# Kernel optimization log

Measured on AMD Instinct MI355X. Metric: run time of the kernel, lower is better.

The kernel has to match this reference:

```python
import jax, jax.numpy as jnp
import numpy as np

N, K, D, H, F = 4, 2048, 512, 8, 2048
Dh = D // H  # per-head dim_q = dim_v = dim_out = 64
EPS = 1e-10


def _uinit(k, shape, fan_sum):
    c = (6.0 / fan_sum) ** 0.5
    return jax.random.uniform(k, shape, jnp.float32, -c, c)


def setup_inputs() -> dict:
    key = jax.random.key(0)
    ks = jax.random.split(key, 8)
    x = jax.random.normal(ks[0], (N, K, D), jnp.float32)
    # per-head projection weights, stacked over heads: (H, D, Dh)
    Wq = _uinit(ks[1], (H, D, Dh), D + Dh)
    Wk = _uinit(ks[2], (H, D, Dh), D + Dh)
    Wv = _uinit(ks[3], (H, D, Dh), D + Dh)
    bq = jnp.zeros((H, Dh), jnp.float32)
    bk = jnp.zeros((H, Dh), jnp.float32)
    bv = jnp.zeros((H, Dh), jnp.float32)
    Wo = _uinit(ks[4], (H * Dh, D), H * Dh + D)
    bo = jnp.zeros((D,), jnp.float32)
    W1 = _uinit(ks[5], (D, F), D + F)
    b1 = jnp.zeros((F,), jnp.float32)
    W2 = _uinit(ks[6], (F, D), F + D)
    b2 = jnp.zeros((D,), jnp.float32)
    g1 = jnp.ones((D,), jnp.float32)
    be1 = jnp.zeros((D,), jnp.float32)
    g2 = jnp.ones((D,), jnp.float32)
    be2 = jnp.zeros((D,), jnp.float32)
    # causal mask: True = masked position (masked_fill semantics)
    mask = jnp.broadcast_to(jnp.triu(jnp.ones((K, K), bool), 1), (N, K, K))
    return dict(x=x, Wq=Wq, bq=bq, Wk=Wk, bk=bk, Wv=Wv, bv=bv, Wo=Wo, bo=bo,
                W1=W1, b1=b1, W2=W2, b2=b2, g1=g1, be1=be1, g2=g2, be2=be2,
                mask=mask)


def _layer_norm(x, g, b):
    m = x.mean(-1, keepdims=True)
    v = ((x - m) ** 2).mean(-1, keepdims=True)
    return g * (x - m) / jnp.sqrt(v + EPS) + b


def _block(x, Wq, bq, Wk, bk, Wv, bv, Wo, bo, W1, b1, W2, b2, g1, be1, g2, be2, mask):
    # per-head projections: (N, H, K, Dh)
    q = jnp.einsum('nkd,hde->nhke', x, Wq) + bq[None, :, None, :]
    k = jnp.einsum('nkd,hde->nhke', x, Wk) + bk[None, :, None, :]
    v = jnp.einsum('nkd,hde->nhke', x, Wv) + bv[None, :, None, :]
    # full score matrix (N, H, K, K) -- faithful to bmm-softmax-bmm
    s = jnp.einsum('nhqe,nhke->nhqk', q, k) / (Dh ** 0.5)
    s = jnp.where(mask[:, None], -1e9, s)
    w = jax.nn.softmax(s, axis=-1)
    att = jnp.einsum('nhqk,nhke->nhqe', w, v)
    att = att.transpose(0, 2, 1, 3).reshape(N, K, H * Dh)  # concat heads
    att = att @ Wo + bo
    h1 = _layer_norm(x + att, g1, be1)
    ff = jax.nn.relu(h1 @ W1 + b1) @ W2 + b2
    return _layer_norm(h1 + ff, g2, be2)


def reference(x, Wq, bq, Wk, bk, Wv, bv, Wo, bo, W1, b1, W2, b2, g1, be1, g2, be2, mask):
    return _block(x, Wq, bq, Wk, bk, Wv, bv, Wo, bo, W1, b1, W2, b2, g1, be1, g2, be2, mask)
```

## Files before the change

kernel.cpp:

```cpp
#include <hip/hip_runtime.h>
#include <cstdint>

typedef unsigned short u16;
typedef __bf16 bf16x8 __attribute__((ext_vector_type(8)));
typedef float f32x4 __attribute__((ext_vector_type(4)));
struct __align__(8) U2 { unsigned x, y; };

#define NEG_INF (-__builtin_inff())

__device__ __forceinline__ u16 f2bf(float f) {
  unsigned u = __builtin_bit_cast(unsigned, f);
  u += 0x7FFFu + ((u >> 16) & 1u);
  return (u16)(u >> 16);
}
__device__ __forceinline__ float bf2f(u16 b) {
  unsigned u = (unsigned)b << 16;
  return __builtin_bit_cast(float, u);
}
__device__ __forceinline__ u16 bfbits(__bf16 x) { return __builtin_bit_cast(u16, x); }
__device__ __forceinline__ unsigned pk2(float a, float b) {
  u16 lo = bfbits((__bf16)a), hi = bfbits((__bf16)b);
  return (unsigned)lo | ((unsigned)hi << 16);
}

__device__ __forceinline__ void async16(u16* dst, const u16* src) {
  __builtin_amdgcn_global_load_lds(
      (__attribute__((address_space(1))) void*)(u16*)src,
      (__attribute__((address_space(3))) void*)dst, 16, 0, 0);
}

__global__ __launch_bounds__(256) void k_prep(const float* __restrict__ Wo,
                                              const float* __restrict__ W1,
                                              const float* __restrict__ W2,
                                              const float* __restrict__ Wq,
                                              const float* __restrict__ Wk,
                                              const float* __restrict__ Wv,
                                              const float* __restrict__ bq,
                                              const float* __restrict__ bk,
                                              const float* __restrict__ bv,
                                              const float* __restrict__ x,
                                              u16* __restrict__ WoT,
                                              u16* __restrict__ W1T,
                                              u16* __restrict__ W2T,
                                              u16* __restrict__ WqkvT,
                                              float* __restrict__ bqkv,
                                              u16* __restrict__ xb) {
  const int b = blockIdx.x, tid = threadIdx.x;
  if (b >= 1542) {
    int i = (b - 1542) * 256 + tid;
    const float4* in = (const float4*)x;
    float4 a = in[2 * i], c = in[2 * i + 1];
    uint4 r;
    r.x = (unsigned)f2bf(a.x) | ((unsigned)f2bf(a.y) << 16);
    r.y = (unsigned)f2bf(a.z) | ((unsigned)f2bf(a.w) << 16);
    r.z = (unsigned)f2bf(c.x) | ((unsigned)f2bf(c.y) << 16);
    r.w = (unsigned)f2bf(c.z) | ((unsigned)f2bf(c.w) << 16);
    ((uint4*)xb)[i] = r;
    return;
  }
  if (b >= 1536) {
    int i = (b - 1536) * 256 + tid;
    int m = i >> 9, r = i & 511;
    const float* B = (m == 0) ? bq : (m == 1) ? bk : bv;
    bqkv[i] = B[r];
    return;
  }
  __shared__ float t[32][65];
  const float* ip;
  u16* op;
  int R, C, r0, c0;
  if (b < 128)      { ip = Wo; op = WoT; R = 512;  C = 512;  c0 = (b & 7) * 64;          r0 = (b >> 3) * 32; }
  else if (b < 640) { int i = b - 128; ip = W1; op = W1T; R = 512;  C = 2048; c0 = (i & 31) * 64; r0 = (i >> 5) * 32; }
  else if (b < 1152){ int i = b - 640; ip = W2; op = W2T; R = 2048; C = 512;  c0 = (i & 7) * 64;  r0 = (i >> 3) * 32; }
  else {
    int i = b - 1152;
    int z = i >> 4;
    const float* W = (z < 8) ? Wq : (z < 16) ? Wk : Wv;
    ip = W + (size_t)(z & 7) * 32768;
    op = WqkvT + (size_t)z * 32768;
    R = 512; C = 64; c0 = 0; r0 = (i & 15) * 32;
  }
  int tx = tid & 63, ty = tid >> 6;
#pragma unroll
  for (int i = 0; i < 32; i += 4)
    t[ty + i][tx] = ip[(size_t)(r0 + ty + i) * C + c0 + tx];
  __syncthreads();
  int cx = tid & 31, cy = tid >> 5;
#pragma unroll
  for (int j = 0; j < 64; j += 8)
    op[(size_t)(c0 + cy + j) * R + r0 + cx] = f2bf(t[cx][cy + j]);
}

template <bool DBUF, int EPI, int BN>
__global__ __launch_bounds__(256) void k_gemm(const u16* __restrict__ A,
                                              const u16* __restrict__ BT,
                                              const float* __restrict__ bias,
                                              u16* __restrict__ Cout,
                                              int M, int N, int Kd) {
  constexpr int HALF = 8192 + BN * 64;
  __shared__ __align__(16) u16 lds[DBUF ? 2 * HALF : HALF];
  constexpr int NFR = BN / 32;
  constexpr int BITER = BN / 32;
  const int tid = threadIdx.x, wid = tid >> 6, lane = tid & 63;
  const int lr = lane & 15, lg = lane >> 4;
  const int wr = wid >> 1, wc = wid & 1;
  const int bid = blockIdx.x;
  const int xcd = bid & 7, local = bid >> 3;
  const int tm = (xcd * 8 + (local & 7)) * 128;
  const int tn = (local >> 3) * BN;

  f32x4 acc[4][NFR] = {};

  const int srow = lane >> 3;
  const int kb = (lane & 7) ^ srow;

  auto STAGE = [&](int buf, int kt) {
    u16* base = lds + buf * HALF;
#pragma unroll
    for (int it = 0; it < 4; ++it) {
      int rid = wid * 4 + it;
      int row = rid * 8 + srow;
      async16(base + rid * 512, A + (size_t)(tm + row) * Kd + kt + kb * 8);
    }
#pragma unroll
    for (int it = 0; it < BITER; ++it) {
      int rid = wid * BITER + it;
      int row = rid * 8 + srow;
      async16(base + 8192 + rid * 512, BT + (size_t)(tn + row) * Kd + kt + kb * 8);
    }
  };

  auto COMPUTE = [&](const char* lp) {
#pragma unroll
    for (int ks = 0; ks < 2; ++ks) {
      const int kbyte = ks * 64 + lg * 16;
      bf16x8 af[4], bfr[NFR];
#pragma unroll
      for (int mi = 0; mi < 4; ++mi) {
        int row = wr * 64 + mi * 16 + lr;
        af[mi] = *(const bf16x8*)(lp + row * 128 + (kbyte ^ ((row & 7) << 4)));
      }
#pragma unroll
      for (int nj = 0; nj < NFR; ++nj) {
        int row = wc * (BN / 2) + nj * 16 + lr;
        bfr[nj] = *(const bf16x8*)(lp + 16384 + row * 128 + (kbyte ^ ((row & 7) << 4)));
      }
#pragma unroll
      for (int mi = 0; mi < 4; ++mi)
#pragma unroll
        for (int nj = 0; nj < NFR; ++nj)
          acc[mi][nj] = __builtin_amdgcn_mfma_f32_16x16x32_bf16(af[mi], bfr[nj], acc[mi][nj], 0, 0, 0);
    }
  };

  const int nkt = Kd >> 6;
  if constexpr (DBUF) {
    STAGE(0, 0);
    for (int ki = 0; ki < nkt; ++ki) {
      __builtin_amdgcn_s_barrier();
      if (ki + 1 < nkt) {
        STAGE((ki + 1) & 1, (ki + 1) << 6);
        if constexpr (BN == 128) asm volatile("s_waitcnt vmcnt(6)" ::: "memory");
        else                     asm volatile("s_waitcnt vmcnt(5)" ::: "memory");
      } else {
        asm volatile("s_waitcnt vmcnt(0)" ::: "memory");
      }
      __builtin_amdgcn_s_barrier();
      __builtin_amdgcn_sched_barrier(0);
      COMPUTE((const char*)(lds + (ki & 1) * HALF));
    }
  } else {
    for (int ki = 0; ki < nkt; ++ki) {
      STAGE(0, ki << 6);
      __syncthreads();
      COMPUTE((const char*)lds);
      __syncthreads();
    }
  }

#pragma unroll
  for (int mi = 0; mi < 4; ++mi)
#pragma unroll
    for (int nj = 0; nj < NFR; ++nj) {
      int col = tn + wc * (BN / 2) + nj * 16 + lr;
      float bv = bias[col];
#pragma unroll
      for (int r = 0; r < 4; ++r) {
        int row = tm + wr * 64 + mi * 16 + lg * 4 + r;
        float v = acc[mi][nj][r] + bv;
        if (EPI == 1) v = v > 0.f ? v : 0.f;
        Cout[(size_t)row * N + col] = f2bf(v);
      }
    }
}

__global__ __launch_bounds__(256) void k_attn(const u16* __restrict__ QKV,
                                              u16* __restrict__ att) {
  __shared__ __align__(16) u16 lds[36864];
  const int lin = blockIdx.x;
  const int L = (lin & 7) * 64 + (lin >> 3);
  const int p = L & 15, nh = L >> 4;
  const int n = nh >> 3, h = nh & 7;
  const int tid = threadIdx.x, wid = tid >> 6, lane = tid & 63;
  const int lr = lane & 15, lg = lane >> 4;
  char* lp = (char*)lds;
  const u16* Qp = QKV + (size_t)(n * 2048) * 1536 + h * 64;
  const u16* Kp = Qp + 512;
  const u16* Vp = Qp + 1024;

  const int vkv = (tid & 31) * 2;
  const int vd0 = (tid >> 5) * 8;
  const int pwb = 65536 + wid * 2048;
  const float C2 = 0.18033688011112042f;
  const float B0 = 14.426950408889634f;

  for (int ph = 0; ph < 2; ++ph) {
    const int qc = (ph == 0) ? p : 31 - p;
    const int ntiles = qc + 1;
    const int qw = qc * 64 + wid * 16;
    const int qa = qw + lr;

    bf16x8 qf[2];
#pragma unroll
    for (int ks = 0; ks < 2; ++ks)
      qf[ks] = *(const bf16x8*)(Qp + (size_t)(qw + lr) * 1536 + ks * 32 + lg * 8);

    f32x4 o[4] = {};
    float lpart = 0.f;

    auto STAGE_K = [&](int t, int b) {
      const int kv0 = t * 64;
#pragma unroll
      for (int it = 0; it < 2; ++it) {
        int c = (wid * 2 + it) * 64 + lane;
        int row = c >> 3, ce = ((c & 7) ^ (row & 7)) * 8;
        async16(&lds[b * 4096 + (wid * 2 + it) * 512],
                Kp + (size_t)(kv0 + row) * 1536 + ce);
      }
    };
    auto VLAND = [&](bf16x8 va, bf16x8 vb, int b) {
#pragma unroll
      for (int jj = 0; jj < 8; ++jj) {
        int d = vd0 + jj;
        unsigned pk = (unsigned)bfbits(va[jj]) | ((unsigned)bfbits(vb[jj]) << 16);
        *(unsigned*)(lp + 32768 + b * 8192 + d * 128 + ((vkv * 2) ^ ((d & 7) << 4))) = pk;
      }
    };
    auto COMPUTE = [&](int t, int b) {
      const int kv0 = t * 64;
      f32x4 s[4] = {};
      __builtin_amdgcn_s_setprio(1);
#pragma unroll
      for (int nj = 0; nj < 4; ++nj) {
        int row = nj * 16 + lr;
#pragma unroll
        for (int ks = 0; ks < 2; ++ks) {
          bf16x8 kf = *(const bf16x8*)(lp + b * 8192 + row * 128 +
                                       ((ks * 64 + lg * 16) ^ ((row & 7) << 4)));
          s[nj] = __builtin_amdgcn_mfma_f32_16x16x32_bf16(kf, qf[ks], s[nj], 0, 0, 0);
        }
      }
      __builtin_amdgcn_s_setprio(0);

      if (t == ntiles - 1) {
#pragma unroll
        for (int nj = 0; nj < 4; ++nj) {
          int kvb = kv0 + nj * 16 + lg * 4;
#pragma unroll
          for (int r = 0; r < 4; ++r)
            if (kvb + r > qa) s[nj][r] = NEG_INF;
        }
      }

      float psum = 0.f;
#pragma unroll
      for (int nj = 0; nj < 4; ++nj)
#pragma unroll
        for (int r = 0; r < 4; ++r) {
          float pv = exp2f(fmaf(s[nj][r], C2, -B0));
          s[nj][r] = pv;
          psum += pv;
        }
      lpart += psum;

#pragma unroll
      for (int nj = 0; nj < 4; ++nj) {
        U2 val;
        val.x = pk2(s[nj][0], s[nj][1]);
        val.y = pk2(s[nj][2], s[nj][3]);
        *(U2*)(lp + pwb + lr * 128 + ((nj * 32 + lg * 8) ^ ((lr & 7) << 4))) = val;
      }

      bf16x8 pa[2];
#pragma unroll
      for (int ks = 0; ks < 2; ++ks)
        pa[ks] = *(const bf16x8*)(lp + pwb + lr * 128 +
                                  ((ks * 64 + lg * 16) ^ ((lr & 7) << 4)));
      __builtin_amdgcn_s_setprio(1);
#pragma unroll
      for (int nd = 0; nd < 4; ++nd) {
        int row = nd * 16 + lr;
#pragma unroll
        for (int ks = 0; ks < 2; ++ks) {
          bf16x8 vf = *(const bf16x8*)(lp + 32768 + b * 8192 + row * 128 +
                                       ((ks * 64 + lg * 16) ^ ((row & 7) << 4)));
          o[nd] = __builtin_amdgcn_mfma_f32_16x16x32_bf16(vf, pa[ks], o[nd], 0, 0, 0);
        }
      }
      __builtin_amdgcn_s_setprio(0);
    };

    STAGE_K(0, 0);
    if (ntiles > 1) STAGE_K(1, 1);
    {
      bf16x8 v0 = *(const bf16x8*)(Vp + (size_t)vkv * 1536 + vd0);
      bf16x8 v1 = *(const bf16x8*)(Vp + (size_t)(vkv + 1) * 1536 + vd0);
      VLAND(v0, v1, 0);
      if (ntiles > 1) {
        bf16x8 v2 = *(const bf16x8*)(Vp + (size_t)(64 + vkv) * 1536 + vd0);
        bf16x8 v3 = *(const bf16x8*)(Vp + (size_t)(64 + vkv + 1) * 1536 + vd0);
        VLAND(v2, v3, 1);
      }
    }
    __syncthreads();

    for (int t = 0; t < ntiles; t += 2) {
      const bool pre0 = (t + 2 < ntiles);
      const bool pre1 = (t + 3 < ntiles);
      bf16x8 va0, vb0, va1, vb1;
      if (pre0) {
        STAGE_K(t + 2, (t + 2) & 3);
        va0 = *(const bf16x8*)(Vp + (size_t)((t + 2) * 64 + vkv) * 1536 + vd0);
        vb0 = *(const bf16x8*)(Vp + (size_t)((t + 2) * 64 + vkv + 1) * 1536 + vd0);
      }
      if (pre1) {
        STAGE_K(t + 3, (t + 3) & 3);
        va1 = *(const bf16x8*)(Vp + (size_t)((t + 3) * 64 + vkv) * 1536 + vd0);
        vb1 = *(const bf16x8*)(Vp + (size_t)((t + 3) * 64 + vkv + 1) * 1536 + vd0);
      }

      COMPUTE(t, t & 3);
      if (t + 1 < ntiles) COMPUTE(t + 1, (t + 1) & 3);

      if (pre0) VLAND(va0, vb0, (t + 2) & 3);
      if (pre1) VLAND(va1, vb1, (t + 3) & 3);
      __syncthreads();
    }

    float lsum = lpart;
    lsum += __shfl_xor(lsum, 16);
    lsum += __shfl_xor(lsum, 32);
    float li = 1.0f / lsum;

    u16* ap = att + (size_t)(n * 2048 + qw + lr) * 512 + h * 64 + lg * 4;
#pragma unroll
    for (int nd = 0; nd < 4; ++nd) {
      U2 val;
      val.x = pk2(o[nd][0] * li, o[nd][1] * li);
      val.y = pk2(o[nd][2] * li, o[nd][3] * li);
      *(U2*)(ap + nd * 16) = val;
    }
  }
}

template <bool XF32>
__global__ __launch_bounds__(256) void k_add_ln(const void* __restrict__ Xp,
                                                const u16* __restrict__ Yb,
                                                const float* __restrict__ gam,
                                                const float* __restrict__ bet,
                                                float* __restrict__ outf,
                                                u16* __restrict__ outb) {
  const int wid = threadIdx.x >> 6, lane = threadIdx.x & 63;
  const size_t row = (size_t)blockIdx.x * 4 + wid;
  float xv[8];
  if constexpr (XF32) {
    const float4* x = (const float4*)((const float*)Xp + row * 512);
    float4 a0 = x[lane], a1 = x[lane + 64];
    xv[0] = a0.x; xv[1] = a0.y; xv[2] = a0.z; xv[3] = a0.w;
    xv[4] = a1.x; xv[5] = a1.y; xv[6] = a1.z; xv[7] = a1.w;
  } else {
    const u16* x = (const u16*)Xp + row * 512;
    U2 x0 = *(const U2*)(x + lane * 4);
    U2 x1 = *(const U2*)(x + 256 + lane * 4);
    xv[0] = bf2f((u16)(x0.x & 0xFFFF)); xv[1] = bf2f((u16)(x0.x >> 16));
    xv[2] = bf2f((u16)(x0.y & 0xFFFF)); xv[3] = bf2f((u16)(x0.y >> 16));
    xv[4] = bf2f((u16)(x1.x & 0xFFFF)); xv[5] = bf2f((u16)(x1.x >> 16));
    xv[6] = bf2f((u16)(x1.y & 0xFFFF)); xv[7] = bf2f((u16)(x1.y >> 16));
  }
  U2 y0 = *(const U2*)(Yb + row * 512 + lane * 4);
  U2 y1 = *(const U2*)(Yb + row * 512 + 256 + lane * 4);
  float v[8];
  v[0] = xv[0] + bf2f((u16)(y0.x & 0xFFFF));
  v[1] = xv[1] + bf2f((u16)(y0.x >> 16));
  v[2] = xv[2] + bf2f((u16)(y0.y & 0xFFFF));
  v[3] = xv[3] + bf2f((u16)(y0.y >> 16));
  v[4] = xv[4] + bf2f((u16)(y1.x & 0xFFFF));
  v[5] = xv[5] + bf2f((u16)(y1.x >> 16));
  v[6] = xv[6] + bf2f((u16)(y1.y & 0xFFFF));
  v[7] = xv[7] + bf2f((u16)(y1.y >> 16));
  float s = 0.f, ss = 0.f;
#pragma unroll
  for (int i = 0; i < 8; ++i) { s += v[i]; ss += v[i] * v[i]; }
#pragma unroll
  for (int m = 1; m < 64; m <<= 1) { s += __shfl_xor(s, m); ss += __shfl_xor(ss, m); }
  float mean = s * (1.f / 512.f);
  float var = ss * (1.f / 512.f) - mean * mean;
  float rstd = rsqrtf(var + 1e-10f);
  float4 g0 = ((const float4*)gam)[lane], g1 = ((const float4*)gam)[lane + 64];
  float4 e0 = ((const float4*)bet)[lane], e1 = ((const float4*)bet)[lane + 64];
  float o[8];
  o[0] = g0.x * (v[0] - mean) * rstd + e0.x;
  o[1] = g0.y * (v[1] - mean) * rstd + e0.y;
  o[2] = g0.z * (v[2] - mean) * rstd + e0.z;
  o[3] = g0.w * (v[3] - mean) * rstd + e0.w;
  o[4] = g1.x * (v[4] - mean) * rstd + e1.x;
  o[5] = g1.y * (v[5] - mean) * rstd + e1.y;
  o[6] = g1.z * (v[6] - mean) * rstd + e1.z;
  o[7] = g1.w * (v[7] - mean) * rstd + e1.w;
  if (outf) {
    float4* of = (float4*)(outf + row * 512);
    float4 w0, w1;
    w0.x = o[0]; w0.y = o[1]; w0.z = o[2]; w0.w = o[3];
    w1.x = o[4]; w1.y = o[5]; w1.z = o[6]; w1.w = o[7];
    of[lane] = w0;
    of[lane + 64] = w1;
  }
  if (outb) {
    u16* ob = outb + row * 512;
    U2 p0, p1;
    p0.x = pk2(o[0], o[1]); p0.y = pk2(o[2], o[3]);
    p1.x = pk2(o[4], o[5]); p1.y = pk2(o[6], o[7]);
    *(U2*)(ob + lane * 4) = p0;
    *(U2*)(ob + 256 + lane * 4) = p1;
  }
}

extern "C" void kernel_launch(void* const* d_in, const int* in_sizes, int n_in,
                              void* d_out, int out_size, void* d_ws, size_t ws_size,
                              hipStream_t stream) {
  const float* x  = (const float*)d_in[0];
  const float* Wq = (const float*)d_in[1];
  const float* bq = (const float*)d_in[2];
  const float* Wk = (const float*)d_in[3];
  const float* bk = (const float*)d_in[4];
  const float* Wv = (const float*)d_in[5];
  const float* bv = (const float*)d_in[6];
  const float* Wo = (const float*)d_in[7];
  const float* bo = (const float*)d_in[8];
  const float* W1 = (const float*)d_in[9];
  const float* b1 = (const float*)d_in[10];
  const float* W2 = (const float*)d_in[11];
  const float* b2 = (const float*)d_in[12];
  const float* g1 = (const float*)d_in[13];
  const float* be1 = (const float*)d_in[14];
  const float* g2 = (const float*)d_in[15];
  const float* be2 = (const float*)d_in[16];

  char* ws = (char*)d_ws;
  u16* xb  = (u16*)(ws + 0);
  u16* h1b = (u16*)(ws + 0);
  u16* WqkvT = (u16*)(ws + (size_t)(8u << 20));
  u16* WoT = WqkvT + 786432;
  u16* W1T = WoT + 262144;
  u16* W2T = W1T + 1048576;
  float* bqkv = (float*)(W2T + 1048576);
  u16* QKV = (u16*)(ws + (size_t)(16u << 20));
  u16* attproj = (u16*)(ws + (size_t)(16u << 20));
  u16* ff1 = (u16*)(ws + (size_t)(16u << 20));
  u16* attb = (u16*)(ws + (size_t)(40u << 20));
  u16* ffn2 = (u16*)(ws + (size_t)(50u << 20));

  k_prep<<<3590, 256, 0, stream>>>(Wo, W1, W2, Wq, Wk, Wv, bq, bk, bv, x,
                                   WoT, W1T, W2T, WqkvT, bqkv, xb);

  k_gemm<true, 0, 128><<<768, 256, 0, stream>>>(xb, WqkvT, bqkv, QKV, 8192, 1536, 512);
  k_attn<<<512, 256, 0, stream>>>(QKV, attb);
  k_gemm<true, 0, 64><<<512, 256, 0, stream>>>(attb, WoT, bo, attproj, 8192, 512, 512);
  k_add_ln<false><<<2048, 256, 0, stream>>>(xb, attproj, g1, be1, nullptr, h1b);
  k_gemm<false, 1, 128><<<1024, 256, 0, stream>>>(h1b, W1T, b1, ff1, 8192, 2048, 512);
  k_gemm<true, 0, 64><<<512, 256, 0, stream>>>(ff1, W2T, b2, ffn2, 8192, 512, 2048);
  k_add_ln<false><<<2048, 256, 0, stream>>>(h1b, ffn2, g2, be2, (float*)d_out, nullptr);
}
```

Before: 158.2 us.

## Use 8-wave attention blocks over 128-row query chunks with XCD-aware head mapping

The attention kernel moves from 4 waves handling two paired 64-row query chunks one after the other to 8 waves that each take 16 query rows of a single 128-row chunk. K/V staging is spread across twice as many threads, and block order is remapped so each XCD handles four whole heads, with the round order reversing chunk size for balance. Masking now covers the last two KV tiles. This shares each K/V tile load across more query rows and aims to improve cache locality, at the cost of a larger LDS footprint and more waves per block.

Measured after the change: 159.8 us. Within noise of the previous version (+1.0%).

```diff
diff --git a/kernel.cpp b/kernel.cpp
--- a/kernel.cpp
+++ b/kernel.cpp
@@ -3,6 +3,7 @@
 
 typedef unsigned short u16;
 typedef __bf16 bf16x8 __attribute__((ext_vector_type(8)));
+typedef __bf16 bf16x4 __attribute__((ext_vector_type(4)));
 typedef float f32x4 __attribute__((ext_vector_type(4)));
 struct __align__(8) U2 { unsigned x, y; };
 
@@ -194,12 +195,15 @@
     }
 }
 
-__global__ __launch_bounds__(256) void k_attn(const u16* __restrict__ QKV,
+__global__ __launch_bounds__(512) void k_attn(const u16* __restrict__ QKV,
                                               u16* __restrict__ att) {
-  __shared__ __align__(16) u16 lds[36864];
+  __shared__ __align__(16) u16 lds[40960];
   const int lin = blockIdx.x;
-  const int L = (lin & 7) * 64 + (lin >> 3);
-  const int p = L & 15, nh = L >> 4;
+  const int xcd = lin & 7, l = lin >> 3;
+  const int rnd = l >> 5, slot = l & 31;
+  const int hl = rnd * 2 + (slot >> 4);
+  const int c = (rnd == 0) ? (slot & 15) : 15 - (slot & 15);
+  const int nh = xcd * 4 + hl;
   const int n = nh >> 3, h = nh & 7;
   const int tid = threadIdx.x, wid = tid >> 6, lane = tid & 63;
   const int lr = lane & 15, lg = lane >> 4;
@@ -209,157 +213,148 @@
   const u16* Vp = Qp + 1024;
 
   const int vkv = (tid & 31) * 2;
-  const int vd0 = (tid >> 5) * 8;
+  const int vd0 = (tid >> 5) * 4;
   const int pwb = 65536 + wid * 2048;
   const float C2 = 0.18033688011112042f;
   const float B0 = 14.426950408889634f;
 
-  for (int ph = 0; ph < 2; ++ph) {
-    const int qc = (ph == 0) ? p : 31 - p;
-    const int ntiles = qc + 1;
-    const int qw = qc * 64 + wid * 16;
-    const int qa = qw + lr;
-
-    bf16x8 qf[2];
+  const int ntiles = 2 * c + 2;
+  const int qw = c * 128 + wid * 16;
+  const int qa = qw + lr;
+
+  bf16x8 qf[2];
+#pragma unroll
+  for (int ks = 0; ks < 2; ++ks)
+    qf[ks] = *(const bf16x8*)(Qp + (size_t)(qw + lr) * 1536 + ks * 32 + lg * 8);
+
+  f32x4 o[4] = {};
+  float lpart = 0.f;
+
+  auto STAGE_K = [&](int t, int b) {
+    const int kv0 = t * 64;
+    int cc = wid * 64 + lane;
+    int row = cc >> 3, ce = ((cc & 7) ^ (row & 7)) * 8;
+    async16(&lds[b * 4096 + wid * 512], Kp + (size_t)(kv0 + row) * 1536 + ce);
+  };
+  auto VLAND = [&](bf16x4 va, bf16x4 vb, int b) {
+#pragma unroll
+    for (int jj = 0; jj < 4; ++jj) {
+      int d = vd0 + jj;
+      unsigned pk = (unsigned)bfbits(va[jj]) | ((unsigned)bfbits(vb[jj]) << 16);
+      *(unsigned*)(lp + 32768 + b * 8192 + d * 128 + ((vkv * 2) ^ ((d & 7) << 4))) = pk;
+    }
+  };
+  auto COMPUTE = [&](int t, int b) {
+    const int kv0 = t * 64;
+    f32x4 s[4] = {};
+    __builtin_amdgcn_s_setprio(1);
+#pragma unroll
+    for (int nj = 0; nj < 4; ++nj) {
+      int row = nj * 16 + lr;
+#pragma unroll
+      for (int ks = 0; ks < 2; ++ks) {
+        bf16x8 kf = *(const bf16x8*)(lp + b * 8192 + row * 128 +
+                                     ((ks * 64 + lg * 16) ^ ((row & 7) << 4)));
+        s[nj] = __builtin_amdgcn_mfma_f32_16x16x32_bf16(kf, qf[ks], s[nj], 0, 0, 0);
+      }
+    }
+    __builtin_amdgcn_s_setprio(0);
+
+    if (t >= ntiles - 2) {
+#pragma unroll
+      for (int nj = 0; nj < 4; ++nj) {
+        int kvb = kv0 + nj * 16 + lg * 4;
+#pragma unroll
+        for (int r = 0; r < 4; ++r)
+          if (kvb + r > qa) s[nj][r] = NEG_INF;
+      }
+    }
+
+    float psum = 0.f;
+#pragma unroll
+    for (int nj = 0; nj < 4; ++nj)
+#pragma unroll
+      for (int r = 0; r < 4; ++r) {
+        float pv = exp2f(fmaf(s[nj][r], C2, -B0));
+        s[nj][r] = pv;
+        psum += pv;
+      }
+    lpart += psum;
+
+#pragma unroll
+    for (int nj = 0; nj < 4; ++nj) {
+      U2 val;
+      val.x = pk2(s[nj][0], s[nj][1]);
+      val.y = pk2(s[nj][2], s[nj][3]);
+      *(U2*)(lp + pwb + lr * 128 + ((nj * 32 + lg * 8) ^ ((lr & 7) << 4))) = val;
+    }
+
+    bf16x8 pa[2];
 #pragma unroll
     for (int ks = 0; ks < 2; ++ks)
-      qf[ks] = *(const bf16x8*)(Qp + (size_t)(qw + lr) * 1536 + ks * 32 + lg * 8);
-
-    f32x4 o[4] = {};
-    float lpart = 0.f;
-
-    auto STAGE_K = [&](int t, int b) {
-      const int kv0 = t * 64;
-#pragma unroll
-      for (int it = 0; it < 2; ++it) {
-        int c = (wid * 2 + it) * 64 + lane;
-        int row = c >> 3, ce = ((c & 7) ^ (row & 7)) * 8;
-        async16(&lds[b * 4096 + (wid * 2 + it) * 512],
-                Kp + (size_t)(kv0 + row) * 1536 + ce);
-      }
-    };
-    auto VLAND = [&](bf16x8 va, bf16x8 vb, int b) {
-#pragma unroll
-      for (int jj = 0; jj < 8; ++jj) {
-        int d = vd0 + jj;
-        unsigned pk = (unsigned)bfbits(va[jj]) | ((unsigned)bfbits(vb[jj]) << 16);
-        *(unsigned*)(lp + 32768 + b * 8192 + d * 128 + ((vkv * 2) ^ ((d & 7) << 4))) = pk;
-      }
-    };
-    auto COMPUTE = [&](int t, int b) {
-      const int kv0 = t * 64;
-      f32x4 s[4] = {};
-      __builtin_amdgcn_s_setprio(1);
-#pragma unroll
-      for (int nj = 0; nj < 4; ++nj) {
-        int row = nj * 16 + lr;
-#pragma unroll
-        for (int ks = 0; ks < 2; ++ks) {
-          bf16x8 kf = *(const bf16x8*)(lp + b * 8192 + row * 128 +
-                                       ((ks * 64 + lg * 16) ^ ((row & 7) << 4)));
-          s[nj] = __builtin_amdgcn_mfma_f32_16x16x32_bf16(kf, qf[ks], s[nj], 0, 0, 0);
-        }
-      }
-      __builtin_amdgcn_s_setprio(0);
-
-      if (t == ntiles - 1) {
-#pragma unroll
-        for (int nj = 0; nj < 4; ++nj) {
-          int kvb = kv0 + nj * 16 + lg * 4;
-#pragma unroll
-          for (int r = 0; r < 4; ++r)
-            if (kvb + r > qa) s[nj][r] = NEG_INF;
-        }
-      }
-
-      float psum = 0.f;
-#pragma unroll
-      for (int nj = 0; nj < 4; ++nj)
-#pragma unroll
-        for (int r = 0; r < 4; ++r) {
-          float pv = exp2f(fmaf(s[nj][r], C2, -B0));
-          s[nj][r] = pv;
-          psum += pv;
-        }
-      lpart += psum;
-
-#pragma unroll
-      for (int nj = 0; nj < 4; ++nj) {
-        U2 val;
-        val.x = pk2(s[nj][0], s[nj][1]);
-        val.y = pk2(s[nj][2], s[nj][3]);
-        *(U2*)(lp + pwb + lr * 128 + ((nj * 32 + lg * 8) ^ ((lr & 7) << 4))) = val;
-      }
-
-      bf16x8 pa[2];
-#pragma unroll
-      for (int ks = 0; ks < 2; ++ks)
-        pa[ks] = *(const bf16x8*)(lp + pwb + lr * 128 +
-                                  ((ks * 64 + lg * 16) ^ ((lr & 7) << 4)));
-      __builtin_amdgcn_s_setprio(1);
-#pragma unroll
-      for (int nd = 0; nd < 4; ++nd) {
-        int row = nd * 16 + lr;
-#pragma unroll
-        for (int ks = 0; ks < 2; ++ks) {
-          bf16x8 vf = *(const bf16x8*)(lp + 32768 + b * 8192 + row * 128 +
-                                       ((ks * 64 + lg * 16) ^ ((row & 7) << 4)));
-          o[nd] = __builtin_amdgcn_mfma_f32_16x16x32_bf16(vf, pa[ks], o[nd], 0, 0, 0);
-        }
-      }
-      __builtin_amdgcn_s_setprio(0);
-    };
-
-    STAGE_K(0, 0);
-    if (ntiles > 1) STAGE_K(1, 1);
-    {
-      bf16x8 v0 = *(const bf16x8*)(Vp + (size_t)vkv * 1536 + vd0);
-      bf16x8 v1 = *(const bf16x8*)(Vp + (size_t)(vkv + 1) * 1536 + vd0);
-      VLAND(v0, v1, 0);
-      if (ntiles > 1) {
-        bf16x8 v2 = *(const bf16x8*)(Vp + (size_t)(64 + vkv) * 1536 + vd0);
-        bf16x8 v3 = *(const bf16x8*)(Vp + (size_t)(64 + vkv + 1) * 1536 + vd0);
-        VLAND(v2, v3, 1);
-      }
-    }
+      pa[ks] = *(const bf16x8*)(lp + pwb + lr * 128 +
+                                ((ks * 64 + lg * 16) ^ ((lr & 7) << 4)));
+    __builtin_amdgcn_s_setprio(1);
+#pragma unroll
+    for (int nd = 0; nd < 4; ++nd) {
+      int row = nd * 16 + lr;
+#pragma unroll
+      for (int ks = 0; ks < 2; ++ks) {
+        bf16x8 vf = *(const bf16x8*)(lp + 32768 + b * 8192 + row * 128 +
+                                     ((ks * 64 + lg * 16) ^ ((row & 7) << 4)));
+        o[nd] = __builtin_amdgcn_mfma_f32_16x16x32_bf16(vf, pa[ks], o[nd], 0, 0, 0);
+      }
+    }
+    __builtin_amdgcn_s_setprio(0);
+  };
+
+  STAGE_K(0, 0);
+  STAGE_K(1, 1);
+  {
+    bf16x4 v0 = *(const bf16x4*)(Vp + (size_t)vkv * 1536 + vd0);
+    bf16x4 v1 = *(const bf16x4*)(Vp + (size_t)(vkv + 1) * 1536 + vd0);
+    VLAND(v0, v1, 0);
+    bf16x4 v2 = *(const bf16x4*)(Vp + (size_t)(64 + vkv) * 1536 + vd0);
+    bf16x4 v3 = *(const bf16x4*)(Vp + (size_t)(64 + vkv + 1) * 1536 + vd0);
+    VLAND(v2, v3, 1);
+  }
+  __syncthreads();
+
+  for (int t = 0; t < ntiles; t += 2) {
+    const bool pre0 = (t + 2 < ntiles);
+    const bool pre1 = (t + 3 < ntiles);
+    bf16x4 va0, vb0, va1, vb1;
+    if (pre0) {
+      STAGE_K(t + 2, (t + 2) & 3);
+      va0 = *(const bf16x4*)(Vp + (size_t)((t + 2) * 64 + vkv) * 1536 + vd0);
+      vb0 = *(const bf16x4*)(Vp + (size_t)((t + 2) * 64 + vkv + 1) * 1536 + vd0);
+    }
+    if (pre1) {
+      STAGE_K(t + 3, (t + 3) & 3);
+      va1 = *(const bf16x4*)(Vp + (size_t)((t + 3) * 64 + vkv) * 1536 + vd0);
+      vb1 = *(const bf16x4*)(Vp + (size_t)((t + 3) * 64 + vkv + 1) * 1536 + vd0);
+    }
+
+    COMPUTE(t, t & 3);
+    COMPUTE(t + 1, (t + 1) & 3);
+
+    if (pre0) VLAND(va0, vb0, (t + 2) & 3);
+    if (pre1) VLAND(va1, vb1, (t + 3) & 3);
     __syncthreads();
-
-    for (int t = 0; t < ntiles; t += 2) {
-      const bool pre0 = (t + 2 < ntiles);
-      const bool pre1 = (t + 3 < ntiles);
-      bf16x8 va0, vb0, va1, vb1;
-      if (pre0) {
-        STAGE_K(t + 2, (t + 2) & 3);
-        va0 = *(const bf16x8*)(Vp + (size_t)((t + 2) * 64 + vkv) * 1536 + vd0);
-        vb0 = *(const bf16x8*)(Vp + (size_t)((t + 2) * 64 + vkv + 1) * 1536 + vd0);
-      }
-      if (pre1) {
-        STAGE_K(t + 3, (t + 3) & 3);
-        va1 = *(const bf16x8*)(Vp + (size_t)((t + 3) * 64 + vkv) * 1536 + vd0);
-        vb1 = *(const bf16x8*)(Vp + (size_t)((t + 3) * 64 + vkv + 1) * 1536 + vd0);
-      }
-
-      COMPUTE(t, t & 3);
-      if (t + 1 < ntiles) COMPUTE(t + 1, (t + 1) & 3);
-
-      if (pre0) VLAND(va0, vb0, (t + 2) & 3);
-      if (pre1) VLAND(va1, vb1, (t + 3) & 3);
-      __syncthreads();
-    }
-
-    float lsum = lpart;
-    lsum += __shfl_xor(lsum, 16);
-    lsum += __shfl_xor(lsum, 32);
-    float li = 1.0f / lsum;
-
-    u16* ap = att + (size_t)(n * 2048 + qw + lr) * 512 + h * 64 + lg * 4;
-#pragma unroll
-    for (int nd = 0; nd < 4; ++nd) {
-      U2 val;
-      val.x = pk2(o[nd][0] * li, o[nd][1] * li);
-      val.y = pk2(o[nd][2] * li, o[nd][3] * li);
-      *(U2*)(ap + nd * 16) = val;
-    }
+  }
+
+  float lsum = lpart;
+  lsum += __shfl_xor(lsum, 16);
+  lsum += __shfl_xor(lsum, 32);
+  float li = 1.0f / lsum;
+
+  u16* ap = att + (size_t)(n * 2048 + qw + lr) * 512 + h * 64 + lg * 4;
+#pragma unroll
+  for (int nd = 0; nd < 4; ++nd) {
+    U2 val;
+    val.x = pk2(o[nd][0] * li, o[nd][1] * li);
+    val.y = pk2(o[nd][2] * li, o[nd][3] * li);
+    *(U2*)(ap + nd * 16) = val;
   }
 }
 
@@ -474,7 +469,7 @@
                                    WoT, W1T, W2T, WqkvT, bqkv, xb);
 
   k_gemm<true, 0, 128><<<768, 256, 0, stream>>>(xb, WqkvT, bqkv, QKV, 8192, 1536, 512);
-  k_attn<<<512, 256, 0, stream>>>(QKV, attb);
+  k_attn<<<512, 512, 0, stream>>>(QKV, attb);
   k_gemm<true, 0, 64><<<512, 256, 0, stream>>>(attb, WoT, bo, attproj, 8192, 512, 512);
   k_add_ln<false><<<2048, 256, 0, stream>>>(xb, attproj, g1, be1, nullptr, h1b);
   k_gemm<false, 1, 128><<<1024, 256, 0, stream>>>(h1b, W1T, b1, ff1, 8192, 2048, 512);
```
